# Kernel tuning notes

Hardware: AMD Instinct MI355X
Metric: run time of the kernel (lower is better)

The kernel has to match this reference:

```python
import jax, jax.numpy as jnp
import numpy as np

DIM = 1024
DIM_HEAD = 64
HEADS = 8
MULT = 4
ATTN_INNER = HEADS * DIM_HEAD            # 512
FF_INNER = MULT * DIM                    # 4096
FUSED = ATTN_INNER + DIM_HEAD + DIM_HEAD + 2 * FF_INNER  # 8832


def setup_inputs() -> dict:
    key = jax.random.key(0)
    ks = jax.random.split(key, 5)
    x = jax.random.normal(ks[0], (2, 2048, DIM), dtype=jnp.float32)
    gamma = jnp.ones((DIM,), dtype=jnp.float32)
    # Linear weights stored as [in, out]
    w_fused = jax.random.normal(ks[1], (DIM, FUSED), dtype=jnp.float32) * (DIM ** -0.5)
    w_attn_out = jax.random.normal(ks[2], (ATTN_INNER, DIM), dtype=jnp.float32) * (ATTN_INNER ** -0.5)
    w_ff_out = jax.random.normal(ks[3], (FF_INNER, DIM), dtype=jnp.float32) * (FF_INNER ** -0.5)
    return {"x": x, "gamma": gamma, "w_fused": w_fused,
            "w_attn_out": w_attn_out, "w_ff_out": w_ff_out}


def _forward(x, gamma, w_fused, w_attn_out, w_ff_out):
    b, n, d = x.shape
    # LayerNorm (beta buffer is zeros)
    mu = jnp.mean(x, axis=-1, keepdims=True)
    var = jnp.mean(jnp.square(x - mu), axis=-1, keepdims=True)
    xn = (x - mu) * jax.lax.rsqrt(var + 1e-5) * gamma
    # fused QKV + FF projection
    proj = jnp.einsum('bnd,df->bnf', xn, w_fused)
    q = proj[..., :ATTN_INNER]
    k = proj[..., ATTN_INNER:ATTN_INNER + DIM_HEAD]
    v = proj[..., ATTN_INNER + DIM_HEAD:ATTN_INNER + 2 * DIM_HEAD]
    ff = proj[..., ATTN_INNER + 2 * DIM_HEAD:]
    # multi-query attention: single shared K/V head of width DIM_HEAD
    q = q.reshape(b, n, HEADS, DIM_HEAD).transpose(0, 2, 1, 3) * (DIM_HEAD ** -0.5)
    sim = jnp.einsum('bhid,bjd->bhij', q, k)
    attn = jax.nn.softmax(sim, axis=-1)
    out = jnp.einsum('bhij,bjd->bhid', attn, v)
    out = out.transpose(0, 2, 1, 3).reshape(b, n, ATTN_INNER)
    attn_out = jnp.einsum('bna,ad->bnd', out, w_attn_out)
    # parallel SwiGLU FF: chunk -> (x_part, gate); silu(gate)*x_part
    ff_x, gate = ff[..., :FF_INNER], ff[..., FF_INNER:]
    ff_out = jnp.einsum('bnf,fd->bnd', jax.nn.silu(gate) * ff_x, w_ff_out)
    return attn_out + ff_out


def reference(x, gamma, w_fused, w_attn_out, w_ff_out):
    return _forward(x, gamma, w_fused, w_attn_out, w_ff_out)
```

## Files before the change

kernel.cpp:

```cpp
#include <hip/hip_runtime.h>
#include <hip/hip_bf16.h>
#include <stdint.h>

#define DIM     1024
#define SEQ     2048
#define NTOK    4096
#define HEADS   8
#define DH      64
#define AINNER  512
#define FFI     4096
#define FUSED   8832
#define HCOLS   4608

typedef __attribute__((ext_vector_type(8))) short short8;
typedef __attribute__((ext_vector_type(4))) short short4v;
typedef __attribute__((ext_vector_type(4))) float f32x4;

__device__ __forceinline__ short f2bf(float f) {
  union { float f; uint32_t u; } v; v.f = f;
  uint32_t r = v.u + 0x7fffu + ((v.u >> 16) & 1u);
  return (short)(r >> 16);
}
__device__ __forceinline__ float bf2f(short s) {
  union { uint32_t u; float f; } v; v.u = ((uint32_t)(uint16_t)s) << 16;
  return v.f;
}
__device__ __forceinline__ void g2l16(const void* g, void* l) {
  __builtin_amdgcn_global_load_lds((const __attribute__((address_space(1))) void*)g,
                                   (__attribute__((address_space(3))) void*)l, 16, 0, 0);
}

__global__ __launch_bounds__(256) void k_transpose_wf(const float* __restrict__ src,
                                                      short* __restrict__ dst) {
  __shared__ short tile[32][33];
  int c0 = blockIdx.x * 32;
  int r0 = blockIdx.y * 32;
  int tx = threadIdx.x & 31, ty = threadIdx.x >> 5;
#pragma unroll
  for (int i = 0; i < 32; i += 8)
    tile[ty + i][tx] = f2bf(src[(size_t)(r0 + ty + i) * FUSED + c0 + tx]);
  __syncthreads();
#pragma unroll
  for (int i = 0; i < 32; i += 8)
    dst[(size_t)(c0 + ty + i) * DIM + r0 + tx] = tile[tx][ty + i];
}

__global__ __launch_bounds__(256) void k_transpose_w2(const float* __restrict__ wao,
                                                      const float* __restrict__ wfo,
                                                      short* __restrict__ dst) {
  __shared__ short tile[32][33];
  int c0 = blockIdx.x * 32;
  int r0 = blockIdx.y * 32;
  int tx = threadIdx.x & 31, ty = threadIdx.x >> 5;
#pragma unroll
  for (int i = 0; i < 32; i += 8) {
    int r = r0 + ty + i;
    float v = (r < AINNER) ? wao[(size_t)r * DIM + c0 + tx]
                           : wfo[(size_t)(r - AINNER) * DIM + c0 + tx];
    tile[ty + i][tx] = f2bf(v);
  }
  __syncthreads();
#pragma unroll
  for (int i = 0; i < 32; i += 8)
    dst[(size_t)(c0 + ty + i) * HCOLS + r0 + tx] = tile[tx][ty + i];
}

__global__ __launch_bounds__(256) void k_ln(const float* __restrict__ x,
                                            const float* __restrict__ gamma,
                                            short* __restrict__ xn) {
  int row = blockIdx.x;
  int t = threadIdx.x;
  const float4* xr = (const float4*)(x + (size_t)row * DIM);
  float4 v = xr[t];
  float s = v.x + v.y + v.z + v.w;
  float s2 = v.x * v.x + v.y * v.y + v.z * v.z + v.w * v.w;
#pragma unroll
  for (int m = 1; m < 64; m <<= 1) { s += __shfl_xor(s, m); s2 += __shfl_xor(s2, m); }
  __shared__ float red[8];
  int w = t >> 6;
  if ((t & 63) == 0) { red[w] = s; red[4 + w] = s2; }
  __syncthreads();
  s = red[0] + red[1] + red[2] + red[3];
  s2 = red[4] + red[5] + red[6] + red[7];
  float mu = s * (1.f / DIM);
  float rs = rsqrtf(s2 * (1.f / DIM) - mu * mu + 1e-5f);
  const float4* g4 = (const float4*)gamma;
  float4 g = g4[t];
  short4v o;
  o.x = f2bf((v.x - mu) * rs * g.x);
  o.y = f2bf((v.y - mu) * rs * g.y);
  o.z = f2bf((v.z - mu) * rs * g.z);
  o.w = f2bf((v.w - mu) * rs * g.w);
  ((short4v*)(xn + (size_t)row * DIM))[t] = o;
}

__global__ __launch_bounds__(512, 2) void p1(const short* __restrict__ A,
                                             const short* __restrict__ Bt,
                                             short* __restrict__ qb,
                                             short* __restrict__ kbf,
                                             short* __restrict__ vtb,
                                             short* __restrict__ H) {
  extern __shared__ __align__(16) short S[];
  int tid = threadIdx.x, l = tid & 63, w = tid >> 6;
  int wm = w >> 2, wn = w & 3;
  int hw = blockIdx.y * 37 + blockIdx.x;
  int tile = (hw & 7) * 74 + (hw >> 3);
  int bx = tile % 37, by = tile / 37;
  int mBase = by * 256;
  bool fused = bx < 32;
  int b0row = fused ? (640 + bx * 128) : ((bx - 32) * 128);
  int b1row = 4736 + bx * 128;

  int srow = w * 8 + (l >> 3);
  int cs = (l & 7) ^ (l >> 3);
  const short* Ag = A + (size_t)(mBase + srow) * DIM + cs * 8;
  const short* Bg0 = Bt + (size_t)(b0row + srow) * DIM + cs * 8;
  const short* Bg1 = Bt + (size_t)(b1row + srow) * DIM + cs * 8;
  int dsto = w * 512 + l * 8;

#define P1_STAGE(kt, db)                                                        \
  {                                                                             \
    _Pragma("unroll") for (int i = 0; i < 4; ++i)                               \
        g2l16(Ag + (size_t)(i * 64) * DIM + (kt) * 64,                          \
              S + (db) * 16384 + i * 4096 + dsto);                              \
    _Pragma("unroll") for (int i = 0; i < 2; ++i)                               \
        g2l16(Bg0 + (size_t)(i * 64) * DIM + (kt) * 64,                         \
              S + 32768 + (db) * 16384 + i * 4096 + dsto);                      \
    if (fused) {                                                                \
      _Pragma("unroll") for (int i = 0; i < 2; ++i)                             \
          g2l16(Bg1 + (size_t)(i * 64) * DIM + (kt) * 64,                       \
                S + 32768 + (db) * 16384 + 8192 + i * 4096 + dsto);             \
    }                                                                           \
  }

  const int NT = DIM / 64;
  P1_STAGE(0, 0);

  int c0 = l & 15, kg = l >> 4, cx = l & 7;
  f32x4 zero = {0.f, 0.f, 0.f, 0.f};
  f32x4 accF[8][2], accG[8][2];
#pragma unroll
  for (int m = 0; m < 8; ++m)
#pragma unroll
    for (int n = 0; n < 2; ++n) { accF[m][n] = zero; accG[m][n] = zero; }

  for (int kt = 0; kt < NT; ++kt) {
    int db = kt & 1, dbn = db ^ 1;
    asm volatile("s_waitcnt vmcnt(0)\ns_barrier" ::: "memory");
    if (kt + 1 < NT) P1_STAGE(kt + 1, dbn);
    const short* Ab = S + db * 16384;
    const short* Bb = S + 32768 + db * 16384;
#pragma unroll
    for (int kkh = 0; kkh < 2; ++kkh) {
      int ch8 = ((kkh * 4 + kg) ^ cx) * 8;
      short8 bf0 = *(const short8*)(Bb + (wn * 32 + c0) * 64 + ch8);
      short8 bf1 = *(const short8*)(Bb + (wn * 32 + 16 + c0) * 64 + ch8);
      if (fused) {
        short8 bg0 = *(const short8*)(Bb + (128 + wn * 32 + c0) * 64 + ch8);
        short8 bg1 = *(const short8*)(Bb + (128 + wn * 32 + 16 + c0) * 64 + ch8);
        __builtin_amdgcn_s_setprio(1);
#pragma unroll
        for (int m = 0; m < 8; ++m) {
          short8 a = *(const short8*)(Ab + (wm * 128 + m * 16 + c0) * 64 + ch8);
          accF[m][0] = __builtin_amdgcn_mfma_f32_16x16x32_bf16(a, bf0, accF[m][0], 0, 0, 0);
          accF[m][1] = __builtin_amdgcn_mfma_f32_16x16x32_bf16(a, bf1, accF[m][1], 0, 0, 0);
          accG[m][0] = __builtin_amdgcn_mfma_f32_16x16x32_bf16(a, bg0, accG[m][0], 0, 0, 0);
          accG[m][1] = __builtin_amdgcn_mfma_f32_16x16x32_bf16(a, bg1, accG[m][1], 0, 0, 0);
        }
        __builtin_amdgcn_s_setprio(0);
      } else {
        __builtin_amdgcn_s_setprio(1);
#pragma unroll
        for (int m = 0; m < 8; ++m) {
          short8 a = *(const short8*)(Ab + (wm * 128 + m * 16 + c0) * 64 + ch8);
          accF[m][0] = __builtin_amdgcn_mfma_f32_16x16x32_bf16(a, bf0, accF[m][0], 0, 0, 0);
          accF[m][1] = __builtin_amdgcn_mfma_f32_16x16x32_bf16(a, bf1, accF[m][1], 0, 0, 0);
        }
        __builtin_amdgcn_s_setprio(0);
      }
    }
  }
#undef P1_STAGE

  int r0 = (l >> 4) * 4;
#pragma unroll
  for (int m = 0; m < 8; ++m)
#pragma unroll
    for (int n = 0; n < 2; ++n)
#pragma unroll
      for (int r = 0; r < 4; ++r) {
        int row = mBase + wm * 128 + m * 16 + r0 + r;
        if (fused) {
          int col = bx * 128 + wn * 32 + n * 16 + c0;
          float g = accG[m][n][r];
          float sg = g / (1.f + __expf(-g));
          H[(size_t)row * HCOLS + AINNER + col] = f2bf(sg * accF[m][n][r]);
        } else {
          int col = (bx - 32) * 128 + wn * 32 + n * 16 + c0;
          float val = accF[m][n][r];
          if (col < AINNER)
            qb[(size_t)row * AINNER + col] = f2bf(val);
          else if (col < AINNER + DH)
            kbf[(size_t)row * DH + (col - AINNER)] = f2bf(val);
          else
            vtb[((size_t)(row >> 11) * DH + (col - AINNER - DH)) * SEQ +
                (row & (SEQ - 1))] = f2bf(val);
        }
      }
}

__global__ __launch_bounds__(512, 2) void gemm_s(const short* __restrict__ A,
                                                 const short* __restrict__ Bt,
                                                 short* __restrict__ part) {
  extern __shared__ __align__(16) short S[];
  int tid = threadIdx.x, l = tid & 63, w = tid >> 6;
  int wm = w >> 2, wn = w & 3;
  int hw = (blockIdx.z * 16 + blockIdx.y) * 4 + blockIdx.x;
  int tile = (hw & 7) * 32 + (hw >> 3);
  int bx = tile & 3, by = (tile >> 2) & 15, bz = tile >> 6;
  int mBase = by * 256, nBase = bx * 256;
  int kOff = bz * 1152;

  int srow = w * 8 + (l >> 3);
  int cs = (l & 7) ^ (l >> 3);
  const short* Ag = A + (size_t)(mBase + srow) * HCOLS + kOff + cs * 8;
  const short* Bg = Bt + (size_t)(nBase + srow) * HCOLS + kOff + cs * 8;
  int dsto = w * 512 + l * 8;

#define GS_STAGE(kt, db)                                                        \
  {                                                                             \
    _Pragma("unroll") for (int i = 0; i < 4; ++i) {                             \
      g2l16(Ag + (size_t)(i * 64) * HCOLS + (kt) * 64,                          \
            S + (db) * 16384 + i * 4096 + dsto);                                \
      g2l16(Bg + (size_t)(i * 64) * HCOLS + (kt) * 64,                          \
            S + 32768 + (db) * 16384 + i * 4096 + dsto);                        \
    }                                                                           \
  }

  const int NT = 18;
  GS_STAGE(0, 0);

  int c0 = l & 15, kg = l >> 4, cx = l & 7;
  f32x4 zero = {0.f, 0.f, 0.f, 0.f};
  f32x4 acc[8][4];
#pragma unroll
  for (int m = 0; m < 8; ++m)
#pragma unroll
    for (int n = 0; n < 4; ++n) acc[m][n] = zero;

  for (int kt = 0; kt < NT; ++kt) {
    int db = kt & 1, dbn = db ^ 1;
    asm volatile("s_waitcnt vmcnt(0)\ns_barrier" ::: "memory");
    if (kt + 1 < NT) GS_STAGE(kt + 1, dbn);
    const short* Ab = S + db * 16384;
    const short* Bb = S + 32768 + db * 16384;
#pragma unroll
    for (int kkh = 0; kkh < 2; ++kkh) {
      int ch8 = ((kkh * 4 + kg) ^ cx) * 8;
      short8 b[4];
#pragma unroll
      for (int n = 0; n < 4; ++n)
        b[n] = *(const short8*)(Bb + (wn * 64 + n * 16 + c0) * 64 + ch8);
      __builtin_amdgcn_s_setprio(1);
#pragma unroll
      for (int m = 0; m < 8; ++m) {
        short8 a = *(const short8*)(Ab + (wm * 128 + m * 16 + c0) * 64 + ch8);
#pragma unroll
        for (int n = 0; n < 4; ++n)
          acc[m][n] = __builtin_amdgcn_mfma_f32_16x16x32_bf16(a, b[n], acc[m][n], 0, 0, 0);
      }
      __builtin_amdgcn_s_setprio(0);
    }
  }
#undef GS_STAGE

  int r0 = (l >> 4) * 4;
#pragma unroll
  for (int m = 0; m < 8; ++m)
#pragma unroll
    for (int n = 0; n < 4; ++n)
#pragma unroll
      for (int r = 0; r < 4; ++r) {
        int row = mBase + wm * 128 + m * 16 + r0 + r;
        int col = nBase + wn * 64 + n * 16 + c0;
        part[(size_t)bz * (NTOK * DIM) + (size_t)row * DIM + col] = f2bf(acc[m][n][r]);
      }
}

__global__ __launch_bounds__(256) void k_red(const short* __restrict__ part,
                                             float* __restrict__ out) {
  int i = (blockIdx.x * 256 + threadIdx.x) * 4;
  float4 s = {0.f, 0.f, 0.f, 0.f};
#pragma unroll
  for (int ks = 0; ks < 4; ++ks) {
    short4v v = *(const short4v*)(part + (size_t)ks * (NTOK * DIM) + i);
    s.x += bf2f(v.x); s.y += bf2f(v.y); s.z += bf2f(v.z); s.w += bf2f(v.w);
  }
  *(float4*)(out + i) = s;
}

__global__ __launch_bounds__(512, 2) void gemm_r(const short* __restrict__ A, int lda,
                                                 const short* __restrict__ Bt, int ldb,
                                                 int K, float* __restrict__ out0) {
  extern __shared__ __align__(16) short SA[];
  int tid = threadIdx.x, l = tid & 63, w = tid >> 6;
  int gx = gridDim.x;
  int nwg = gx * gridDim.y;
  int hw = blockIdx.y * gx + blockIdx.x;
  int qq = nwg >> 3;
  int tile = (hw & 7) * qq + (hw >> 3);
  int bx = tile % gx, by = tile / gx;
  int mBase = by * 128, nBase = bx * 128;

  int srow = w * 8 + (l >> 3);
  int cs = (l & 7) ^ (l >> 3);
  const short* Ag = A + (size_t)(mBase + srow) * lda + cs * 8;
  const short* Bg = Bt + (size_t)(nBase + srow) * ldb + cs * 8;
  short* ldsA = SA + w * 512 + l * 8;
  short* ldsB = ldsA + 8192;

  int NT = K >> 6;
  for (int tt = 0; tt < 3; ++tt) {
    int slot = tt & 3;
#pragma unroll
    for (int i = 0; i < 2; ++i) {
      g2l16(Ag + (size_t)(i * 64) * lda + tt * 64, ldsA + slot * 16384 + i * 4096);
      g2l16(Bg + (size_t)(i * 64) * ldb + tt * 64, ldsB + slot * 16384 + i * 4096);
    }
  }

  int wr = w >> 2, wc = w & 3;
  int c0 = l & 15, kg = l >> 4, cx = l & 7;
  f32x4 zero = {0.f, 0.f, 0.f, 0.f};
  f32x4 acc[4][2];
#pragma unroll
  for (int m = 0; m < 4; ++m)
#pragma unroll
    for (int n = 0; n < 2; ++n) acc[m][n] = zero;

  for (int kt = 0; kt < NT; ++kt) {
    if (kt + 2 < NT)      asm volatile("s_waitcnt vmcnt(8)\ns_barrier" ::: "memory");
    else if (kt + 1 < NT) asm volatile("s_waitcnt vmcnt(4)\ns_barrier" ::: "memory");
    else                  asm volatile("s_waitcnt vmcnt(0)\ns_barrier" ::: "memory");
    int slot = kt & 3;
    const short* Ab = SA + slot * 16384;
    const short* Bb = Ab + 8192;
    short8 af[4][2], bfr[2][2];
#pragma unroll
    for (int m = 0; m < 4; ++m)
#pragma unroll
      for (int kk = 0; kk < 2; ++kk)
        af[m][kk] = *(const short8*)(Ab + (wr * 64 + m * 16 + c0) * 64 + ((kk * 4 + kg) ^ cx) * 8);
#pragma unroll
    for (int n = 0; n < 2; ++n)
#pragma unroll
      for (int kk = 0; kk < 2; ++kk)
        bfr[n][kk] = *(const short8*)(Bb + (wc * 32 + n * 16 + c0) * 64 + ((kk * 4 + kg) ^ cx) * 8);
    int ts = kt + 3;
    if (ts < NT) {
      int s2 = ts & 3;
#pragma unroll
      for (int i = 0; i < 2; ++i) {
        g2l16(Ag + (size_t)(i * 64) * lda + ts * 64, ldsA + s2 * 16384 + i * 4096);
        g2l16(Bg + (size_t)(i * 64) * ldb + ts * 64, ldsB + s2 * 16384 + i * 4096);
      }
    }
    __builtin_amdgcn_s_setprio(1);
#pragma unroll
    for (int m = 0; m < 4; ++m)
#pragma unroll
      for (int n = 0; n < 2; ++n)
#pragma unroll
        for (int kk = 0; kk < 2; ++kk)
          acc[m][n] = __builtin_amdgcn_mfma_f32_16x16x32_bf16(af[m][kk], bfr[n][kk],
                                                              acc[m][n], 0, 0, 0);
    __builtin_amdgcn_s_setprio(0);
  }

  int r0 = (l >> 4) * 4;
#pragma unroll
  for (int m = 0; m < 4; ++m)
#pragma unroll
    for (int n = 0; n < 2; ++n)
#pragma unroll
      for (int r = 0; r < 4; ++r) {
        int row = mBase + wr * 64 + m * 16 + r0 + r;
        int col = nBase + wc * 32 + n * 16 + c0;
        out0[(size_t)row * DIM + col] = acc[m][n][r];
      }
}

__global__ __launch_bounds__(256) void k_attn(const short* __restrict__ qb,
                                              const short* __restrict__ kb,
                                              const short* __restrict__ vt,
                                              short* __restrict__ H) {
  __shared__ __align__(16) short Qs[64 * 64];
  __shared__ __align__(16) short Ks[128 * 64];
  __shared__ __align__(16) short Vs[64 * 128];
  __shared__ __align__(16) short Ps[4][16 * 128];
  int t = threadIdx.x, l = t & 63, w = t >> 6;
  int qt = blockIdx.x, bh = blockIdx.y;
  int b = bh >> 3, h = bh & 7;
  int q0 = qt * 64;

  int srow = w * 8 + (l >> 3);
  int schunk = (l & 7) ^ (l >> 3);
  {
    const short* Qg = qb + (size_t)(b * SEQ + q0 + srow) * AINNER + h * DH + schunk * 8;
    short* qs = Qs + w * 512 + l * 8;
#pragma unroll
    for (int i = 0; i < 2; ++i) g2l16(Qg + (size_t)(i * 32) * AINNER, qs + i * 2048);
  }
  const short* Kg = kb + (size_t)(b * SEQ + srow) * DH + schunk * 8;
  short* ksl = Ks + w * 512 + l * 8;
  int vrow = w * 4 + (l >> 4);
  int vchunk = (l & 15) ^ (vrow & 7);
  const short* Vg = vt + (size_t)b * DH * SEQ + (size_t)vrow * SEQ + vchunk * 8;
  short* vsl = Vs + w * 512 + l * 8;

#pragma unroll
  for (int i = 0; i < 4; ++i) {
    g2l16(Kg + (size_t)(i * 32) * DH, ksl + i * 2048);
    g2l16(Vg + (size_t)(i * 16) * SEQ, vsl + i * 2048);
  }

  float m_run[4], l_run[4];
  f32x4 zero = {0.f, 0.f, 0.f, 0.f};
  f32x4 Oacc[4];
#pragma unroll
  for (int r = 0; r < 4; ++r) { m_run[r] = -1e30f; l_run[r] = 0.f; }
#pragma unroll
  for (int n = 0; n < 4; ++n) Oacc[n] = zero;

  int c0 = l & 15, kg = l >> 4, cx = l & 7;
  short* pw = Ps[w];

  for (int kv0 = 0; kv0 < SEQ; kv0 += 128) {
    asm volatile("s_waitcnt vmcnt(0)\ns_barrier" ::: "memory");

    f32x4 sacc[8];
#pragma unroll
    for (int n = 0; n < 8; ++n) sacc[n] = zero;
#pragma unroll
    for (int kk = 0; kk < 2; ++kk) {
      int rr = w * 16 + c0;
      short8 aq = *(const short8*)(Qs + rr * 64 + ((kk * 4 + kg) ^ cx) * 8);
#pragma unroll
      for (int n = 0; n < 8; ++n) {
        int kr = n * 16 + c0;
        short8 bk = *(const short8*)(Ks + kr * 64 + ((kk * 4 + kg) ^ cx) * 8);
        sacc[n] = __builtin_amdgcn_mfma_f32_16x16x32_bf16(aq, bk, sacc[n], 0, 0, 0);
      }
    }
#pragma unroll
    for (int r = 0; r < 4; ++r) {
      float mx = -1e30f;
#pragma unroll
      for (int n = 0; n < 8; ++n) {
        sacc[n][r] *= 0.125f;
        mx = fmaxf(mx, sacc[n][r]);
      }
#pragma unroll
      for (int msk = 1; msk < 16; msk <<= 1) mx = fmaxf(mx, __shfl_xor(mx, msk));
      float nm = fmaxf(m_run[r], mx);
      float corr = __expf(m_run[r] - nm);
      m_run[r] = nm;
      float rs = 0.f;
#pragma unroll
      for (int n = 0; n < 8; ++n) {
        float p = __expf(sacc[n][r] - nm);
        sacc[n][r] = p;
        rs += p;
      }
#pragma unroll
      for (int msk = 1; msk < 16; msk <<= 1) rs += __shfl_xor(rs, msk);
      l_run[r] = l_run[r] * corr + rs;
      Oacc[0][r] *= corr; Oacc[1][r] *= corr; Oacc[2][r] *= corr; Oacc[3][r] *= corr;
    }
#pragma unroll
    for (int n = 0; n < 8; ++n)
#pragma unroll
      for (int r = 0; r < 4; ++r) {
        int pr = (l >> 4) * 4 + r;
        int pc = n * 16 + c0;
        pw[pr * 128 + ((pc >> 3) ^ (pr & 7)) * 8 + (pc & 7)] = f2bf(sacc[n][r]);
      }
    asm volatile("s_waitcnt lgkmcnt(0)" ::: "memory");
#pragma unroll
    for (int kk = 0; kk < 4; ++kk) {
      int pr = c0;
      short8 ap = *(const short8*)(pw + pr * 128 + ((kk * 4 + kg) ^ cx) * 8);
#pragma unroll
      for (int n = 0; n < 4; ++n) {
        int vr = n * 16 + c0;
        short8 bv = *(const short8*)(Vs + vr * 128 + ((kk * 4 + kg) ^ (vr & 7)) * 8);
        Oacc[n] = __builtin_amdgcn_mfma_f32_16x16x32_bf16(ap, bv, Oacc[n], 0, 0, 0);
      }
    }
    __syncthreads();
    int nx = kv0 + 128;
    if (nx < SEQ) {
#pragma unroll
      for (int i = 0; i < 4; ++i) {
        g2l16(Kg + (size_t)(nx + i * 32) * DH, ksl + i * 2048);
        g2l16(Vg + nx + (size_t)(i * 16) * SEQ, vsl + i * 2048);
      }
    }
  }
#pragma unroll
  for (int r = 0; r < 4; ++r) {
    float inv = 1.f / l_run[r];
    int row = b * SEQ + q0 + w * 16 + (l >> 4) * 4 + r;
#pragma unroll
    for (int n = 0; n < 4; ++n) {
      int col = h * DH + n * 16 + c0;
      H[(size_t)row * HCOLS + col] = f2bf(Oacc[n][r] * inv);
    }
  }
}

extern "C" void kernel_launch(void* const* d_in, const int* in_sizes, int n_in,
                              void* d_out, int out_size, void* d_ws, size_t ws_size,
                              hipStream_t stream) {
  const float* x     = (const float*)d_in[0];
  const float* gamma = (const float*)d_in[1];
  const float* w_f   = (const float*)d_in[2];
  const float* w_ao  = (const float*)d_in[3];
  const float* w_fo  = (const float*)d_in[4];
  float* out = (float*)d_out;

  char* ws = (char*)d_ws;
  size_t o = 0;
  short* WtF = (short*)(ws + o); o += (size_t)FUSED * DIM * 2;
  short* Wt2 = (short*)(ws + o); o += (size_t)DIM * HCOLS * 2;
  short* xn  = (short*)(ws + o); o += (size_t)NTOK * DIM * 2;
  short* qb  = (short*)(ws + o); o += (size_t)NTOK * AINNER * 2;
  short* kbf = (short*)(ws + o); o += (size_t)NTOK * DH * 2;
  short* vtb = (short*)(ws + o); o += (size_t)NTOK * DH * 2;
  short* H   = (short*)(ws + o); o += (size_t)NTOK * HCOLS * 2;
  short* part = (short*)(ws + o);
  size_t need = o + (size_t)4 * NTOK * DIM * 2;

  k_transpose_wf<<<dim3(FUSED / 32, DIM / 32), 256, 0, stream>>>(w_f, WtF);
  k_transpose_w2<<<dim3(DIM / 32, HCOLS / 32), 256, 0, stream>>>(w_ao, w_fo, Wt2);
  k_ln<<<NTOK, 256, 0, stream>>>(x, gamma, xn);
  p1<<<dim3(37, 16), 512, 131072, stream>>>(xn, WtF, qb, kbf, vtb, H);
  k_attn<<<dim3(32, 16), 256, 0, stream>>>(qb, kbf, vtb, H);
  if (ws_size >= need) {
    gemm_s<<<dim3(4, 16, 4), 512, 131072, stream>>>(H, Wt2, part);
    k_red<<<NTOK * DIM / 1024, 256, 0, stream>>>(part, out);
  } else {
    gemm_r<<<dim3(8, 32), 512, 131072, stream>>>(H, HCOLS, Wt2, HCOLS, HCOLS, out);
  }
}
```

Baseline: 223.4 us.

## Split GEMM K-step into four quadrant phases with staggered loads and partial waits

Restructures the fused p1 path and the split-K gemm_s kernel so each warp computes four 64x32 quadrant sub-tiles per K-step. Global-to-LDS loads for the next stage are issued in four pieces interleaved between quadrant MFMA phases, gated by partial vmcnt waits, instead of one full wait and barrier per step. The intent is to overlap memory traffic with MFMA work and reduce register pressure from fragment reuse. It also removes the gemm_r fallback and always uses the split-K path, which assumes the workspace is large enough.

```diff
diff --git a/kernel.cpp b/kernel.cpp
--- a/kernel.cpp
+++ b/kernel.cpp
@@ -29,6 +29,11 @@
   __builtin_amdgcn_global_load_lds((const __attribute__((address_space(1))) void*)g,
                                    (__attribute__((address_space(3))) void*)l, 16, 0, 0);
 }
+
+#define PH_W4 asm volatile("s_waitcnt vmcnt(4)\ns_barrier" ::: "memory")
+#define PH_W2 asm volatile("s_waitcnt vmcnt(2)\ns_barrier" ::: "memory")
+#define PH_W0 asm volatile("s_waitcnt vmcnt(0)\ns_barrier" ::: "memory")
+#define PH_B  asm volatile("s_barrier" ::: "memory")
 
 __global__ __launch_bounds__(256) void k_transpose_wf(const float* __restrict__ src,
                                                       short* __restrict__ dst) {
@@ -102,7 +107,6 @@
                                              short* __restrict__ H) {
   extern __shared__ __align__(16) short S[];
   int tid = threadIdx.x, l = tid & 63, w = tid >> 6;
-  int wm = w >> 2, wn = w & 3;
   int hw = blockIdx.y * 37 + blockIdx.x;
   int tile = (hw & 7) * 74 + (hw >> 3);
   int bx = tile % 37, by = tile / 37;
@@ -118,86 +122,57 @@
   const short* Bg1 = Bt + (size_t)(b1row + srow) * DIM + cs * 8;
   int dsto = w * 512 + l * 8;
 
-#define P1_STAGE(kt, db)                                                        \
-  {                                                                             \
-    _Pragma("unroll") for (int i = 0; i < 4; ++i)                               \
-        g2l16(Ag + (size_t)(i * 64) * DIM + (kt) * 64,                          \
-              S + (db) * 16384 + i * 4096 + dsto);                              \
-    _Pragma("unroll") for (int i = 0; i < 2; ++i)                               \
-        g2l16(Bg0 + (size_t)(i * 64) * DIM + (kt) * 64,                         \
-              S + 32768 + (db) * 16384 + i * 4096 + dsto);                      \
-    if (fused) {                                                                \
-      _Pragma("unroll") for (int i = 0; i < 2; ++i)                             \
-          g2l16(Bg1 + (size_t)(i * 64) * DIM + (kt) * 64,                       \
-                S + 32768 + (db) * 16384 + 8192 + i * 4096 + dsto);             \
-    }                                                                           \
-  }
+#define STG_A0(kt, db) { _Pragma("unroll") for (int i = 0; i < 2; ++i) \
+    g2l16(Ag + (size_t)(i * 64) * DIM + (kt) * 64, S + (db) * 16384 + i * 4096 + dsto); }
+#define STG_A1(kt, db) { _Pragma("unroll") for (int i = 2; i < 4; ++i) \
+    g2l16(Ag + (size_t)(i * 64) * DIM + (kt) * 64, S + (db) * 16384 + i * 4096 + dsto); }
+#define STG_B0(kt, db) { _Pragma("unroll") for (int i = 0; i < 2; ++i) \
+    g2l16(Bg0 + (size_t)(i * 64) * DIM + (kt) * 64, S + 32768 + (db) * 16384 + i * 4096 + dsto); }
+#define STG_B1(kt, db) { _Pragma("unroll") for (int i = 0; i < 2; ++i) \
+    g2l16(Bg1 + (size_t)(i * 64) * DIM + (kt) * 64, S + 32768 + (db) * 16384 + 8192 + i * 4096 + dsto); }
 
   const int NT = DIM / 64;
-  P1_STAGE(0, 0);
-
   int c0 = l & 15, kg = l >> 4, cx = l & 7;
+  int ch0 = (kg ^ cx) * 8, ch1 = ((4 + kg) ^ cx) * 8;
+  int r0 = (l >> 4) * 4;
   f32x4 zero = {0.f, 0.f, 0.f, 0.f};
-  f32x4 accF[8][2], accG[8][2];
-#pragma unroll
-  for (int m = 0; m < 8; ++m)
-#pragma unroll
-    for (int n = 0; n < 2; ++n) { accF[m][n] = zero; accG[m][n] = zero; }
-
-  for (int kt = 0; kt < NT; ++kt) {
-    int db = kt & 1, dbn = db ^ 1;
-    asm volatile("s_waitcnt vmcnt(0)\ns_barrier" ::: "memory");
-    if (kt + 1 < NT) P1_STAGE(kt + 1, dbn);
-    const short* Ab = S + db * 16384;
-    const short* Bb = S + 32768 + db * 16384;
-#pragma unroll
-    for (int kkh = 0; kkh < 2; ++kkh) {
-      int ch8 = ((kkh * 4 + kg) ^ cx) * 8;
-      short8 bf0 = *(const short8*)(Bb + (wn * 32 + c0) * 64 + ch8);
-      short8 bf1 = *(const short8*)(Bb + (wn * 32 + 16 + c0) * 64 + ch8);
-      if (fused) {
-        short8 bg0 = *(const short8*)(Bb + (128 + wn * 32 + c0) * 64 + ch8);
-        short8 bg1 = *(const short8*)(Bb + (128 + wn * 32 + 16 + c0) * 64 + ch8);
+
+  if (!fused) {
+    STG_A0(0, 0); STG_A1(0, 0); STG_B0(0, 0);
+    int wm = w >> 2, wn = w & 3;
+    f32x4 acc[8][2];
+#pragma unroll
+    for (int m = 0; m < 8; ++m) { acc[m][0] = zero; acc[m][1] = zero; }
+    for (int kt = 0; kt < NT; ++kt) {
+      int db = kt & 1, dbn = db ^ 1;
+      PH_W0;
+      if (kt + 1 < NT) { STG_A0(kt + 1, dbn); STG_A1(kt + 1, dbn); STG_B0(kt + 1, dbn); }
+      const short* Ab = S + db * 16384;
+      const short* Bb = S + 32768 + db * 16384;
+#pragma unroll
+      for (int kkh = 0; kkh < 2; ++kkh) {
+        int ch8 = kkh ? ch1 : ch0;
+        short8 b0 = *(const short8*)(Bb + (wn * 32 + c0) * 64 + ch8);
+        short8 b1 = *(const short8*)(Bb + (wn * 32 + 16 + c0) * 64 + ch8);
         __builtin_amdgcn_s_setprio(1);
 #pragma unroll
         for (int m = 0; m < 8; ++m) {
           short8 a = *(const short8*)(Ab + (wm * 128 + m * 16 + c0) * 64 + ch8);
-          accF[m][0] = __builtin_amdgcn_mfma_f32_16x16x32_bf16(a, bf0, accF[m][0], 0, 0, 0);
-          accF[m][1] = __builtin_amdgcn_mfma_f32_16x16x32_bf16(a, bf1, accF[m][1], 0, 0, 0);
-          accG[m][0] = __builtin_amdgcn_mfma_f32_16x16x32_bf16(a, bg0, accG[m][0], 0, 0, 0);
-          accG[m][1] = __builtin_amdgcn_mfma_f32_16x16x32_bf16(a, bg1, accG[m][1], 0, 0, 0);
+          acc[m][0] = __builtin_amdgcn_mfma_f32_16x16x32_bf16(a, b0, acc[m][0], 0, 0, 0);
+          acc[m][1] = __builtin_amdgcn_mfma_f32_16x16x32_bf16(a, b1, acc[m][1], 0, 0, 0);
         }
         __builtin_amdgcn_s_setprio(0);
-      } else {
-        __builtin_amdgcn_s_setprio(1);
-#pragma unroll
-        for (int m = 0; m < 8; ++m) {
-          short8 a = *(const short8*)(Ab + (wm * 128 + m * 16 + c0) * 64 + ch8);
-          accF[m][0] = __builtin_amdgcn_mfma_f32_16x16x32_bf16(a, bf0, accF[m][0], 0, 0, 0);
-          accF[m][1] = __builtin_amdgcn_mfma_f32_16x16x32_bf16(a, bf1, accF[m][1], 0, 0, 0);
-        }
-        __builtin_amdgcn_s_setprio(0);
-      }
-    }
-  }
-#undef P1_STAGE
-
-  int r0 = (l >> 4) * 4;
-#pragma unroll
-  for (int m = 0; m < 8; ++m)
-#pragma unroll
-    for (int n = 0; n < 2; ++n)
-#pragma unroll
-      for (int r = 0; r < 4; ++r) {
-        int row = mBase + wm * 128 + m * 16 + r0 + r;
-        if (fused) {
-          int col = bx * 128 + wn * 32 + n * 16 + c0;
-          float g = accG[m][n][r];
-          float sg = g / (1.f + __expf(-g));
-          H[(size_t)row * HCOLS + AINNER + col] = f2bf(sg * accF[m][n][r]);
-        } else {
+      }
+    }
+#pragma unroll
+    for (int m = 0; m < 8; ++m)
+#pragma unroll
+      for (int n = 0; n < 2; ++n)
+#pragma unroll
+        for (int r = 0; r < 4; ++r) {
+          float val = acc[m][n][r];
+          int row = mBase + wm * 128 + m * 16 + r0 + r;
           int col = (bx - 32) * 128 + wn * 32 + n * 16 + c0;
-          float val = accF[m][n][r];
           if (col < AINNER)
             qb[(size_t)row * AINNER + col] = f2bf(val);
           else if (col < AINNER + DH)
@@ -206,7 +181,111 @@
             vtb[((size_t)(row >> 11) * DH + (col - AINNER - DH)) * SEQ +
                 (row & (SEQ - 1))] = f2bf(val);
         }
-      }
+    return;
+  }
+
+  STG_A0(0, 0); STG_B0(0, 0); STG_B1(0, 0); STG_A1(0, 0);
+  int ra = (w >> 2) * 64, rb = (w & 3) * 32;
+  f32x4 acc[2][2][4][2];
+#pragma unroll
+  for (int a = 0; a < 2; ++a)
+#pragma unroll
+    for (int b = 0; b < 2; ++b)
+#pragma unroll
+      for (int m = 0; m < 4; ++m)
+#pragma unroll
+        for (int n = 0; n < 2; ++n) acc[a][b][m][n] = zero;
+
+  for (int kt = 0; kt < NT; ++kt) {
+    int db = kt & 1, dbn = db ^ 1;
+    bool st = kt + 1 < NT;
+    const short* Ab = S + db * 16384;
+    const short* Bb = S + 32768 + db * 16384;
+    short8 aF[4][2], bF[2][2], bG[2][2];
+    PH_W4;
+#pragma unroll
+    for (int m = 0; m < 4; ++m) {
+      aF[m][0] = *(const short8*)(Ab + (ra + m * 16 + c0) * 64 + ch0);
+      aF[m][1] = *(const short8*)(Ab + (ra + m * 16 + c0) * 64 + ch1);
+    }
+#pragma unroll
+    for (int n = 0; n < 2; ++n) {
+      bF[n][0] = *(const short8*)(Bb + (rb + n * 16 + c0) * 64 + ch0);
+      bF[n][1] = *(const short8*)(Bb + (rb + n * 16 + c0) * 64 + ch1);
+    }
+    if (st) STG_A0(kt + 1, dbn);
+    __builtin_amdgcn_s_setprio(1);
+#pragma unroll
+    for (int m = 0; m < 4; ++m)
+#pragma unroll
+      for (int n = 0; n < 2; ++n) {
+        acc[0][0][m][n] = __builtin_amdgcn_mfma_f32_16x16x32_bf16(aF[m][0], bF[n][0], acc[0][0][m][n], 0, 0, 0);
+        acc[0][0][m][n] = __builtin_amdgcn_mfma_f32_16x16x32_bf16(aF[m][1], bF[n][1], acc[0][0][m][n], 0, 0, 0);
+      }
+    __builtin_amdgcn_s_setprio(0);
+    if (st) PH_W4; else PH_W2;
+#pragma unroll
+    for (int n = 0; n < 2; ++n) {
+      bG[n][0] = *(const short8*)(Bb + 8192 + (rb + n * 16 + c0) * 64 + ch0);
+      bG[n][1] = *(const short8*)(Bb + 8192 + (rb + n * 16 + c0) * 64 + ch1);
+    }
+    if (st) STG_B0(kt + 1, dbn);
+    __builtin_amdgcn_s_setprio(1);
+#pragma unroll
+    for (int m = 0; m < 4; ++m)
+#pragma unroll
+      for (int n = 0; n < 2; ++n) {
+        acc[0][1][m][n] = __builtin_amdgcn_mfma_f32_16x16x32_bf16(aF[m][0], bG[n][0], acc[0][1][m][n], 0, 0, 0);
+        acc[0][1][m][n] = __builtin_amdgcn_mfma_f32_16x16x32_bf16(aF[m][1], bG[n][1], acc[0][1][m][n], 0, 0, 0);
+      }
+    __builtin_amdgcn_s_setprio(0);
+    if (st) PH_W4; else PH_W0;
+#pragma unroll
+    for (int m = 0; m < 4; ++m) {
+      aF[m][0] = *(const short8*)(Ab + 8192 + (ra + m * 16 + c0) * 64 + ch0);
+      aF[m][1] = *(const short8*)(Ab + 8192 + (ra + m * 16 + c0) * 64 + ch1);
+    }
+    if (st) STG_B1(kt + 1, dbn);
+    __builtin_amdgcn_s_setprio(1);
+#pragma unroll
+    for (int m = 0; m < 4; ++m)
+#pragma unroll
+      for (int n = 0; n < 2; ++n) {
+        acc[1][1][m][n] = __builtin_amdgcn_mfma_f32_16x16x32_bf16(aF[m][0], bG[n][0], acc[1][1][m][n], 0, 0, 0);
+        acc[1][1][m][n] = __builtin_amdgcn_mfma_f32_16x16x32_bf16(aF[m][1], bG[n][1], acc[1][1][m][n], 0, 0, 0);
+      }
+    __builtin_amdgcn_s_setprio(0);
+    PH_B;
+    if (st) STG_A1(kt + 1, dbn);
+    __builtin_amdgcn_s_setprio(1);
+#pragma unroll
+    for (int m = 0; m < 4; ++m)
+#pragma unroll
+      for (int n = 0; n < 2; ++n) {
+        acc[1][0][m][n] = __builtin_amdgcn_mfma_f32_16x16x32_bf16(aF[m][0], bF[n][0], acc[1][0][m][n], 0, 0, 0);
+        acc[1][0][m][n] = __builtin_amdgcn_mfma_f32_16x16x32_bf16(aF[m][1], bF[n][1], acc[1][0][m][n], 0, 0, 0);
+      }
+    __builtin_amdgcn_s_setprio(0);
+  }
+#undef STG_A0
+#undef STG_A1
+#undef STG_B0
+#undef STG_B1
+
+#pragma unroll
+  for (int a = 0; a < 2; ++a)
+#pragma unroll
+    for (int m = 0; m < 4; ++m)
+#pragma unroll
+      for (int n = 0; n < 2; ++n)
+#pragma unroll
+        for (int r = 0; r < 4; ++r) {
+          int row = mBase + a * 128 + ra + m * 16 + r0 + r;
+          int col = bx * 128 + rb + n * 16 + c0;
+          float g = acc[a][1][m][n][r];
+          float sg = g / (1.f + __expf(-g));
+          H[(size_t)row * HCOLS + AINNER + col] = f2bf(sg * acc[a][0][m][n][r]);
+        }
 }
 
 __global__ __launch_bounds__(512, 2) void gemm_s(const short* __restrict__ A,
@@ -214,7 +293,6 @@
                                                  short* __restrict__ part) {
   extern __shared__ __align__(16) short S[];
   int tid = threadIdx.x, l = tid & 63, w = tid >> 6;
-  int wm = w >> 2, wn = w & 3;
   int hw = (blockIdx.z * 16 + blockIdx.y) * 4 + blockIdx.x;
   int tile = (hw & 7) * 32 + (hw >> 3);
   int bx = tile & 3, by = (tile >> 2) & 15, bz = tile >> 6;
@@ -227,64 +305,123 @@
   const short* Bg = Bt + (size_t)(nBase + srow) * HCOLS + kOff + cs * 8;
   int dsto = w * 512 + l * 8;
 
-#define GS_STAGE(kt, db)                                                        \
-  {                                                                             \
-    _Pragma("unroll") for (int i = 0; i < 4; ++i) {                             \
-      g2l16(Ag + (size_t)(i * 64) * HCOLS + (kt) * 64,                          \
-            S + (db) * 16384 + i * 4096 + dsto);                                \
-      g2l16(Bg + (size_t)(i * 64) * HCOLS + (kt) * 64,                          \
-            S + 32768 + (db) * 16384 + i * 4096 + dsto);                        \
-    }                                                                           \
-  }
+#define SG_A0(kt, db) { _Pragma("unroll") for (int i = 0; i < 2; ++i) \
+    g2l16(Ag + (size_t)(i * 64) * HCOLS + (kt) * 64, S + (db) * 16384 + i * 4096 + dsto); }
+#define SG_A1(kt, db) { _Pragma("unroll") for (int i = 2; i < 4; ++i) \
+    g2l16(Ag + (size_t)(i * 64) * HCOLS + (kt) * 64, S + (db) * 16384 + i * 4096 + dsto); }
+#define SG_B0(kt, db) { _Pragma("unroll") for (int i = 0; i < 2; ++i) \
+    g2l16(Bg + (size_t)(i * 64) * HCOLS + (kt) * 64, S + 32768 + (db) * 16384 + i * 4096 + dsto); }
+#define SG_B1(kt, db) { _Pragma("unroll") for (int i = 2; i < 4; ++i) \
+    g2l16(Bg + (size_t)(i * 64) * HCOLS + (kt) * 64, S + 32768 + (db) * 16384 + i * 4096 + dsto); }
 
   const int NT = 18;
-  GS_STAGE(0, 0);
+  SG_A0(0, 0); SG_B0(0, 0); SG_B1(0, 0); SG_A1(0, 0);
 
   int c0 = l & 15, kg = l >> 4, cx = l & 7;
+  int ch0 = (kg ^ cx) * 8, ch1 = ((4 + kg) ^ cx) * 8;
+  int ra = (w >> 2) * 64, rb = (w & 3) * 32;
   f32x4 zero = {0.f, 0.f, 0.f, 0.f};
-  f32x4 acc[8][4];
-#pragma unroll
-  for (int m = 0; m < 8; ++m)
-#pragma unroll
-    for (int n = 0; n < 4; ++n) acc[m][n] = zero;
+  f32x4 acc[2][2][4][2];
+#pragma unroll
+  for (int a = 0; a < 2; ++a)
+#pragma unroll
+    for (int b = 0; b < 2; ++b)
+#pragma unroll
+      for (int m = 0; m < 4; ++m)
+#pragma unroll
+        for (int n = 0; n < 2; ++n) acc[a][b][m][n] = zero;
 
   for (int kt = 0; kt < NT; ++kt) {
     int db = kt & 1, dbn = db ^ 1;
-    asm volatile("s_waitcnt vmcnt(0)\ns_barrier" ::: "memory");
-    if (kt + 1 < NT) GS_STAGE(kt + 1, dbn);
+    bool st = kt + 1 < NT;
     const short* Ab = S + db * 16384;
     const short* Bb = S + 32768 + db * 16384;
-#pragma unroll
-    for (int kkh = 0; kkh < 2; ++kkh) {
-      int ch8 = ((kkh * 4 + kg) ^ cx) * 8;
-      short8 b[4];
-#pragma unroll
-      for (int n = 0; n < 4; ++n)
-        b[n] = *(const short8*)(Bb + (wn * 64 + n * 16 + c0) * 64 + ch8);
-      __builtin_amdgcn_s_setprio(1);
-#pragma unroll
-      for (int m = 0; m < 8; ++m) {
-        short8 a = *(const short8*)(Ab + (wm * 128 + m * 16 + c0) * 64 + ch8);
-#pragma unroll
-        for (int n = 0; n < 4; ++n)
-          acc[m][n] = __builtin_amdgcn_mfma_f32_16x16x32_bf16(a, b[n], acc[m][n], 0, 0, 0);
-      }
-      __builtin_amdgcn_s_setprio(0);
-    }
-  }
-#undef GS_STAGE
+    short8 aF[4][2], bF[2][2], bG[2][2];
+    PH_W4;
+#pragma unroll
+    for (int m = 0; m < 4; ++m) {
+      aF[m][0] = *(const short8*)(Ab + (ra + m * 16 + c0) * 64 + ch0);
+      aF[m][1] = *(const short8*)(Ab + (ra + m * 16 + c0) * 64 + ch1);
+    }
+#pragma unroll
+    for (int n = 0; n < 2; ++n) {
+      bF[n][0] = *(const short8*)(Bb + (rb + n * 16 + c0) * 64 + ch0);
+      bF[n][1] = *(const short8*)(Bb + (rb + n * 16 + c0) * 64 + ch1);
+    }
+    if (st) SG_A0(kt + 1, dbn);
+    __builtin_amdgcn_s_setprio(1);
+#pragma unroll
+    for (int m = 0; m < 4; ++m)
+#pragma unroll
+      for (int n = 0; n < 2; ++n) {
+        acc[0][0][m][n] = __builtin_amdgcn_mfma_f32_16x16x32_bf16(aF[m][0], bF[n][0], acc[0][0][m][n], 0, 0, 0);
+        acc[0][0][m][n] = __builtin_amdgcn_mfma_f32_16x16x32_bf16(aF[m][1], bF[n][1], acc[0][0][m][n], 0, 0, 0);
+      }
+    __builtin_amdgcn_s_setprio(0);
+    if (st) PH_W4; else PH_W2;
+#pragma unroll
+    for (int n = 0; n < 2; ++n) {
+      bG[n][0] = *(const short8*)(Bb + 8192 + (rb + n * 16 + c0) * 64 + ch0);
+      bG[n][1] = *(const short8*)(Bb + 8192 + (rb + n * 16 + c0) * 64 + ch1);
+    }
+    if (st) SG_B0(kt + 1, dbn);
+    __builtin_amdgcn_s_setprio(1);
+#pragma unroll
+    for (int m = 0; m < 4; ++m)
+#pragma unroll
+      for (int n = 0; n < 2; ++n) {
+        acc[0][1][m][n] = __builtin_amdgcn_mfma_f32_16x16x32_bf16(aF[m][0], bG[n][0], acc[0][1][m][n], 0, 0, 0);
+        acc[0][1][m][n] = __builtin_amdgcn_mfma_f32_16x16x32_bf16(aF[m][1], bG[n][1], acc[0][1][m][n], 0, 0, 0);
+      }
+    __builtin_amdgcn_s_setprio(0);
+    if (st) PH_W4; else PH_W0;
+#pragma unroll
+    for (int m = 0; m < 4; ++m) {
+      aF[m][0] = *(const short8*)(Ab + 8192 + (ra + m * 16 + c0) * 64 + ch0);
+      aF[m][1] = *(const short8*)(Ab + 8192 + (ra + m * 16 + c0) * 64 + ch1);
+    }
+    if (st) SG_B1(kt + 1, dbn);
+    __builtin_amdgcn_s_setprio(1);
+#pragma unroll
+    for (int m = 0; m < 4; ++m)
+#pragma unroll
+      for (int n = 0; n < 2; ++n) {
+        acc[1][1][m][n] = __builtin_amdgcn_mfma_f32_16x16x32_bf16(aF[m][0], bG[n][0], acc[1][1][m][n], 0, 0, 0);
+        acc[1][1][m][n] = __builtin_amdgcn_mfma_f32_16x16x32_bf16(aF[m][1], bG[n][1], acc[1][1][m][n], 0, 0, 0);
+      }
+    __builtin_amdgcn_s_setprio(0);
+    PH_B;
+    if (st) SG_A1(kt + 1, dbn);
+    __builtin_amdgcn_s_setprio(1);
+#pragma unroll
+    for (int m = 0; m < 4; ++m)
+#pragma unroll
+      for (int n = 0; n < 2; ++n) {
+        acc[1][0][m][n] = __builtin_amdgcn_mfma_f32_16x16x32_bf16(aF[m][0], bF[n][0], acc[1][0][m][n], 0, 0, 0);
+        acc[1][0][m][n] = __builtin_amdgcn_mfma_f32_16x16x32_bf16(aF[m][1], bF[n][1], acc[1][0][m][n], 0, 0, 0);
+      }
+    __builtin_amdgcn_s_setprio(0);
+  }
+#undef SG_A0
+#undef SG_A1
+#undef SG_B0
+#undef SG_B1
 
   int r0 = (l >> 4) * 4;
 #pragma unroll
-  for (int m = 0; m < 8; ++m)
-#pragma unroll
-    for (int n = 0; n < 4; ++n)
-#pragma unroll
-      for (int r = 0; r < 4; ++r) {
-        int row = mBase + wm * 128 + m * 16 + r0 + r;
-        int col = nBase + wn * 64 + n * 16 + c0;
-        part[(size_t)bz * (NTOK * DIM) + (size_t)row * DIM + col] = f2bf(acc[m][n][r]);
-      }
+  for (int a = 0; a < 2; ++a)
+#pragma unroll
+    for (int b = 0; b < 2; ++b)
+#pragma unroll
+      for (int m = 0; m < 4; ++m)
+#pragma unroll
+        for (int n = 0; n < 2; ++n)
+#pragma unroll
+          for (int r = 0; r < 4; ++r) {
+            int row = mBase + a * 128 + ra + m * 16 + r0 + r;
+            int col = nBase + b * 128 + rb + n * 16 + c0;
+            part[(size_t)bz * (NTOK * DIM) + (size_t)row * DIM + col] = f2bf(acc[a][b][m][n][r]);
+          }
 }
 
 __global__ __launch_bounds__(256) void k_red(const short* __restrict__ part,
@@ -297,97 +434,6 @@
     s.x += bf2f(v.x); s.y += bf2f(v.y); s.z += bf2f(v.z); s.w += bf2f(v.w);
   }
   *(float4*)(out + i) = s;
-}
-
-__global__ __launch_bounds__(512, 2) void gemm_r(const short* __restrict__ A, int lda,
-                                                 const short* __restrict__ Bt, int ldb,
-                                                 int K, float* __restrict__ out0) {
-  extern __shared__ __align__(16) short SA[];
-  int tid = threadIdx.x, l = tid & 63, w = tid >> 6;
-  int gx = gridDim.x;
-  int nwg = gx * gridDim.y;
-  int hw = blockIdx.y * gx + blockIdx.x;
-  int qq = nwg >> 3;
-  int tile = (hw & 7) * qq + (hw >> 3);
-  int bx = tile % gx, by = tile / gx;
-  int mBase = by * 128, nBase = bx * 128;
-
-  int srow = w * 8 + (l >> 3);
-  int cs = (l & 7) ^ (l >> 3);
-  const short* Ag = A + (size_t)(mBase + srow) * lda + cs * 8;
-  const short* Bg = Bt + (size_t)(nBase + srow) * ldb + cs * 8;
-  short* ldsA = SA + w * 512 + l * 8;
-  short* ldsB = ldsA + 8192;
-
-  int NT = K >> 6;
-  for (int tt = 0; tt < 3; ++tt) {
-    int slot = tt & 3;
-#pragma unroll
-    for (int i = 0; i < 2; ++i) {
-      g2l16(Ag + (size_t)(i * 64) * lda + tt * 64, ldsA + slot * 16384 + i * 4096);
-      g2l16(Bg + (size_t)(i * 64) * ldb + tt * 64, ldsB + slot * 16384 + i * 4096);
-    }
-  }
-
-  int wr = w >> 2, wc = w & 3;
-  int c0 = l & 15, kg = l >> 4, cx = l & 7;
-  f32x4 zero = {0.f, 0.f, 0.f, 0.f};
-  f32x4 acc[4][2];
-#pragma unroll
-  for (int m = 0; m < 4; ++m)
-#pragma unroll
-    for (int n = 0; n < 2; ++n) acc[m][n] = zero;
-
-  for (int kt = 0; kt < NT; ++kt) {
-    if (kt + 2 < NT)      asm volatile("s_waitcnt vmcnt(8)\ns_barrier" ::: "memory");
-    else if (kt + 1 < NT) asm volatile("s_waitcnt vmcnt(4)\ns_barrier" ::: "memory");
-    else                  asm volatile("s_waitcnt vmcnt(0)\ns_barrier" ::: "memory");
-    int slot = kt & 3;
-    const short* Ab = SA + slot * 16384;
-    const short* Bb = Ab + 8192;
-    short8 af[4][2], bfr[2][2];
-#pragma unroll
-    for (int m = 0; m < 4; ++m)
-#pragma unroll
-      for (int kk = 0; kk < 2; ++kk)
-        af[m][kk] = *(const short8*)(Ab + (wr * 64 + m * 16 + c0) * 64 + ((kk * 4 + kg) ^ cx) * 8);
-#pragma unroll
-    for (int n = 0; n < 2; ++n)
-#pragma unroll
-      for (int kk = 0; kk < 2; ++kk)
-        bfr[n][kk] = *(const short8*)(Bb + (wc * 32 + n * 16 + c0) * 64 + ((kk * 4 + kg) ^ cx) * 8);
-    int ts = kt + 3;
-    if (ts < NT) {
-      int s2 = ts & 3;
-#pragma unroll
-      for (int i = 0; i < 2; ++i) {
-        g2l16(Ag + (size_t)(i * 64) * lda + ts * 64, ldsA + s2 * 16384 + i * 4096);
-        g2l16(Bg + (size_t)(i * 64) * ldb + ts * 64, ldsB + s2 * 16384 + i * 4096);
-      }
-    }
-    __builtin_amdgcn_s_setprio(1);
-#pragma unroll
-    for (int m = 0; m < 4; ++m)
-#pragma unroll
-      for (int n = 0; n < 2; ++n)
-#pragma unroll
-        for (int kk = 0; kk < 2; ++kk)
-          acc[m][n] = __builtin_amdgcn_mfma_f32_16x16x32_bf16(af[m][kk], bfr[n][kk],
-                                                              acc[m][n], 0, 0, 0);
-    __builtin_amdgcn_s_setprio(0);
-  }
-
-  int r0 = (l >> 4) * 4;
-#pragma unroll
-  for (int m = 0; m < 4; ++m)
-#pragma unroll
-    for (int n = 0; n < 2; ++n)
-#pragma unroll
-      for (int r = 0; r < 4; ++r) {
-        int row = mBase + wr * 64 + m * 16 + r0 + r;
-        int col = nBase + wc * 32 + n * 16 + c0;
-        out0[(size_t)row * DIM + col] = acc[m][n][r];
-      }
 }
 
 __global__ __launch_bounds__(256) void k_attn(const short* __restrict__ qb,
@@ -539,17 +585,12 @@
   short* vtb = (short*)(ws + o); o += (size_t)NTOK * DH * 2;
   short* H   = (short*)(ws + o); o += (size_t)NTOK * HCOLS * 2;
   short* part = (short*)(ws + o);
-  size_t need = o + (size_t)4 * NTOK * DIM * 2;
 
   k_transpose_wf<<<dim3(FUSED / 32, DIM / 32), 256, 0, stream>>>(w_f, WtF);
   k_transpose_w2<<<dim3(DIM / 32, HCOLS / 32), 256, 0, stream>>>(w_ao, w_fo, Wt2);
   k_ln<<<NTOK, 256, 0, stream>>>(x, gamma, xn);
   p1<<<dim3(37, 16), 512, 131072, stream>>>(xn, WtF, qb, kbf, vtb, H);
   k_attn<<<dim3(32, 16), 256, 0, stream>>>(qb, kbf, vtb, H);
-  if (ws_size >= need) {
-    gemm_s<<<dim3(4, 16, 4), 512, 131072, stream>>>(H, Wt2, part);
-    k_red<<<NTOK * DIM / 1024, 256, 0, stream>>>(part, out);
-  } else {
-    gemm_r<<<dim3(8, 32), 512, 131072, stream>>>(H, HCOLS, Wt2, HCOLS, HCOLS, out);
-  }
-}
+  gemm_s<<<dim3(4, 16, 4), 512, 131072, stream>>>(H, Wt2, part);
+  k_red<<<NTOK * DIM / 1024, 256, 0, stream>>>(part, out);
+}
```

Result: faster. 211.7 us (-5.2%).
